# Kernel tuning notes

Measured on AMD Instinct MI355X. Metric: run time of the kernel, lower is better.

## Reference

```python
import jax, jax.numpy as jnp
import numpy as np

D_MODEL = 1024
NUM_HEADS = 16
D_HEAD = D_MODEL // NUM_HEADS
NEG_BIG = 10000000000.0  # matches the torch module's -1e10 mask constant


def setup_inputs() -> dict:
    key = jax.random.key(0)
    ks = jax.random.split(key, 9)
    d = D_MODEL
    scale = 1.0 / np.sqrt(d)
    inp = {
        "x": jax.random.normal(ks[0], (2, 2048, d), dtype=jnp.float32),
        "W_q": jax.random.normal(ks[1], (d, d), dtype=jnp.float32) * scale,
        "b_q": jnp.zeros((d,), dtype=jnp.float32),
        "W_k": jax.random.normal(ks[2], (d, d), dtype=jnp.float32) * scale,
        "b_k": jnp.zeros((d,), dtype=jnp.float32),
        "W_v": jax.random.normal(ks[3], (d, d), dtype=jnp.float32) * scale,
        "b_v": jnp.zeros((d,), dtype=jnp.float32),
        "W_o": jax.random.normal(ks[4], (d, d), dtype=jnp.float32) * scale,
        "b_o": jnp.zeros((d,), dtype=jnp.float32),
    }
    return inp


def reference(x, W_q, b_q, W_k, b_k, W_v, b_v, W_o, b_o):
    B, S, d = x.shape
    H, Dh = NUM_HEADS, D_HEAD

    Q = x @ W_q + b_q  # [B,S,d]
    K = x @ W_k + b_k
    V = x @ W_v + b_v

    # split heads: [B,S,d] -> [B,H,S,Dh]
    Qh = Q.reshape(B, S, H, Dh).transpose(0, 2, 1, 3)
    Kh = K.reshape(B, S, H, Dh).transpose(0, 2, 1, 3)
    Vh = V.reshape(B, S, H, Dh).transpose(0, 2, 1, 3)

    scores = jnp.einsum("bhid,bhjd->bhij", Qh, Kh) / jnp.sqrt(
        jnp.asarray(Dh, dtype=x.dtype)
    )

    # causal mask: tril(scores) - 1e10 * (1 - tril_mask)
    causal = jnp.tril(jnp.ones((S, S), dtype=x.dtype))
    scores = scores * causal - NEG_BIG * (1.0 - causal)

    attn = jax.nn.softmax(scores, axis=-1)  # dropout p=0.0 -> identity

    vals = jnp.einsum("bhij,bhjd->bhid", attn, Vh)  # [B,H,S,Dh]
    vals = vals.transpose(0, 2, 1, 3).reshape(B, S, d)

    return vals @ W_o + b_o
```

## Files before the change

### kernel.cpp

```cpp
#include <hip/hip_runtime.h>

typedef unsigned short u16;
typedef __attribute__((ext_vector_type(8))) short short8;
typedef __attribute__((ext_vector_type(4))) short shortx4;
typedef __attribute__((ext_vector_type(4))) float floatx4;

#define S_ 2048
#define D_ 1024
#define DQKV_ 3072
#define H_ 16
#define DH_ 64

#define EXP2F(x) __builtin_amdgcn_exp2f(x)

__device__ __forceinline__ float bf2f(u16 x) {
    union { unsigned int u; float f; } v; v.u = ((unsigned int)x) << 16; return v.f;
}
__device__ __forceinline__ u16 f2bf(float f) {
    unsigned int u = __float_as_uint(f);
    return (u16)((u + 0x7fffu + ((u >> 16) & 1u)) >> 16);
}
__device__ __forceinline__ u16 f2bf_fast(float f) {
    return (u16)((__float_as_uint(f) + 0x8000u) >> 16);
}

__device__ __forceinline__ void async16(const void* g, void* l) {
    __builtin_amdgcn_global_load_lds(
        (const __attribute__((address_space(1))) unsigned int*)g,
        (__attribute__((address_space(3))) unsigned int*)l, 16, 0, 0);
}

__global__ __launch_bounds__(256) void convert_x(const float* __restrict__ x, u16* __restrict__ xb) {
    const size_t i = ((size_t)blockIdx.x * 256 + threadIdx.x) * 4;
    float4 v = *(const float4*)&x[i];
    shortx4 h;
    h[0] = (short)f2bf(v.x); h[1] = (short)f2bf(v.y);
    h[2] = (short)f2bf(v.z); h[3] = (short)f2bf(v.w);
    *(shortx4*)&xb[i] = h;
}

__global__ __launch_bounds__(256) void transpose_w4(const float* __restrict__ Wq, const float* __restrict__ Wk,
                                                    const float* __restrict__ Wv, const float* __restrict__ Wo,
                                                    u16* __restrict__ Wqkvt, u16* __restrict__ Wot) {
    __shared__ u16 tile[32][33];
    const int z = blockIdx.z;
    const float* W = (z == 0) ? Wq : (z == 1) ? Wk : (z == 2) ? Wv : Wo;
    u16* dst = (z == 3) ? Wot : (Wqkvt + (size_t)z * D_ * D_);
    const int tx = threadIdx.x, ty = threadIdx.y;
    const int n0 = blockIdx.x * 32, k0 = blockIdx.y * 32;
#pragma unroll
    for (int r = 0; r < 4; ++r) {
        int k = ty + r * 8;
        tile[k][tx] = f2bf(W[(size_t)(k0 + k) * D_ + n0 + tx]);
    }
    __syncthreads();
#pragma unroll
    for (int r = 0; r < 4; ++r) {
        int n = ty + r * 8;
        dst[(size_t)(n0 + n) * D_ + k0 + tx] = tile[tx][n];
    }
}

__global__ __launch_bounds__(256) void transpose_headV(const u16* __restrict__ QKV, u16* __restrict__ Vt) {
    __shared__ u16 tile[64 * 65];
    const int t = threadIdx.x;
    const int bh = blockIdx.y, b = bh >> 4, h = bh & 15;
    const int s0 = blockIdx.x << 6;
#pragma unroll
    for (int i = 0; i < 16; ++i) {
        int idx = t + (i << 8);
        int s = idx >> 6, d = idx & 63;
        tile[s * 65 + d] = QKV[(size_t)(b * S_ + s0 + s) * DQKV_ + 2048 + h * DH_ + d];
    }
    __syncthreads();
#pragma unroll
    for (int i = 0; i < 16; ++i) {
        int idx = t + (i << 8);
        int d = idx >> 6, s = idx & 63;
        Vt[((size_t)bh * DH_ + d) * S_ + s0 + s] = tile[s * 65 + d];
    }
}

template <int BM, int BN, bool OUTF32>
__global__ __launch_bounds__(256) void gemm_bt(const u16* __restrict__ A, const u16* __restrict__ Bt,
                                               const float* __restrict__ b0, const float* __restrict__ b1,
                                               const float* __restrict__ b2, void* __restrict__ Cp,
                                               int M, int N, int Kd) {
    constexpr int FI = BM / 32, FJ = BN / 32;
    __shared__ __align__(16) u16 As[2][BM * 32];
    __shared__ __align__(16) u16 Bs[2][BN * 32];
    const int t = threadIdx.x;
    const int m0 = blockIdx.y * BM, n0 = blockIdx.x * BN;
    const int w = t >> 6, lane = t & 63;
    const int lr = lane & 15, lg = lane >> 4;
    const int wm = (w >> 1) * (BM / 2), wn = (w & 1) * (BN / 2);
    const int srow = lane >> 2, scol = (lane & 3) << 3;
    floatx4 acc[FI][FJ] = {};

    auto stage = [&](int buf, int k0) {
#pragma unroll
        for (int c = 0; c < BM / 64; ++c) {
            int rbase = (w * (BM / 64) + c) * 16;
            async16(&A[(size_t)(m0 + rbase + srow) * Kd + k0 + scol], &As[buf][rbase * 32]);
        }
#pragma unroll
        for (int c = 0; c < BN / 64; ++c) {
            int rbase = (w * (BN / 64) + c) * 16;
            async16(&Bt[(size_t)(n0 + rbase + srow) * Kd + k0 + scol], &Bs[buf][rbase * 32]);
        }
    };

    stage(0, 0);
    const int nk = Kd / 32;
    for (int kk = 0; kk < nk; ++kk) {
        const int cur = kk & 1;
        __syncthreads();
        if (kk + 1 < nk) stage(cur ^ 1, (kk + 1) * 32);

        short8 af[FI], bfr[FJ];
#pragma unroll
        for (int i = 0; i < FI; ++i) af[i]  = *(const short8*)&As[cur][(wm + i * 16 + lr) * 32 + lg * 8];
#pragma unroll
        for (int j = 0; j < FJ; ++j) bfr[j] = *(const short8*)&Bs[cur][(wn + j * 16 + lr) * 32 + lg * 8];
#pragma unroll
        for (int i = 0; i < FI; ++i)
#pragma unroll
            for (int j = 0; j < FJ; ++j)
                acc[i][j] = __builtin_amdgcn_mfma_f32_16x16x32_bf16(af[i], bfr[j], acc[i][j], 0, 0, 0);
    }

#pragma unroll
    for (int j = 0; j < FJ; ++j) {
        int col = n0 + wn + j * 16 + lr;
        const float* bp = (col < 1024) ? b0 : (col < 2048) ? b1 : b2;
        float bv = bp[col & 1023];
#pragma unroll
        for (int i = 0; i < FI; ++i) {
            int rb = m0 + wm + i * 16 + lg * 4;
#pragma unroll
            for (int ii = 0; ii < 4; ++ii) {
                float val = acc[i][j][ii] + bv;
                if (OUTF32) ((float*)Cp)[(size_t)(rb + ii) * N + col] = val;
                else        ((u16*)Cp)[(size_t)(rb + ii) * N + col] = f2bf(val);
            }
        }
    }
}

__global__ __launch_bounds__(256) void attn_mfma(const u16* __restrict__ QKV, const u16* __restrict__ Vt,
                                                 u16* __restrict__ O) {
    __shared__ __align__(16) u16 KsA[2][64 * 64];
    __shared__ __align__(16) u16 VsA[2][64 * 64];
    __shared__ __align__(16) u16 Ps[4 * 16 * 64];
    const int t = threadIdx.x, w = t >> 6, lane = t & 63;
    const int lr = lane & 15, lg = lane >> 4;
    const int bh = blockIdx.x, b = bh >> 4, h = bh & 15;
    const int qt = 31 - blockIdx.y;
    const int q0 = qt << 6;
    const float cs = 0.18033688f;

    const u16* Kb  = QKV + (size_t)b * S_ * DQKV_ + 1024 + h * DH_;
    const u16* Vtb = Vt + (size_t)bh * DH_ * S_;
    u16* Pw = Ps + w * (16 * 64);

    const int rb = lane >> 3;
    const int cc = ((lane & 7) ^ rb) << 3;
    const int swz = lr & 7;

    short8 qf[2];
#pragma unroll
    for (int ks = 0; ks < 2; ++ks)
        qf[ks] = *(const short8*)&QKV[(size_t)(b * S_ + q0 + w * 16 + lr) * DQKV_ + h * DH_ + ks * 32 + lg * 8];

    floatx4 of[4] = {};
    float lsum[4] = {0.f, 0.f, 0.f, 0.f};

    {
        u16* Kd = &KsA[0][w * 512];
        u16* Vd = &VsA[0][w * 512];
        async16(&Kb[(size_t)(w * 8 + rb) * DQKV_ + cc], Kd);
        async16(&Kb[(size_t)(32 + w * 8 + rb) * DQKV_ + cc], Kd + 2048);
        async16(&Vtb[(size_t)(w * 8 + rb) * S_ + cc], Vd);
        async16(&Vtb[(size_t)(32 + w * 8 + rb) * S_ + cc], Vd + 2048);
    }

    for (int kb = 0; kb <= qt; ++kb) {
        const int cur = kb & 1;
        __syncthreads();
        if (kb < qt) {
            const int K1 = (kb + 1) << 6;
            u16* Kd = &KsA[cur ^ 1][w * 512];
            u16* Vd = &VsA[cur ^ 1][w * 512];
            async16(&Kb[(size_t)(K1 + w * 8 + rb) * DQKV_ + cc], Kd);
            async16(&Kb[(size_t)(K1 + 32 + w * 8 + rb) * DQKV_ + cc], Kd + 2048);
            async16(&Vtb[(size_t)(w * 8 + rb) * S_ + K1 + cc], Vd);
            async16(&Vtb[(size_t)(32 + w * 8 + rb) * S_ + K1 + cc], Vd + 2048);
        }
        const u16* Kc = KsA[cur];
        const u16* Vc = VsA[cur];

        floatx4 sf[4] = {};
#pragma unroll
        for (int ks = 0; ks < 2; ++ks)
#pragma unroll
            for (int j = 0; j < 4; ++j) {
                short8 kf = *(const short8*)&Kc[(j * 16 + lr) * 64 + ((((ks << 2) + lg) ^ swz) << 3)];
                sf[j] = __builtin_amdgcn_mfma_f32_16x16x32_bf16(qf[ks], kf, sf[j], 0, 0, 0);
            }

        const bool diag = (kb == qt);
#pragma unroll
        for (int j = 0; j < 4; ++j)
#pragma unroll
            for (int ii = 0; ii < 4; ++ii) {
                float ev = EXP2F(sf[j][ii] * cs);
                if (diag && (j * 16 + lr > w * 16 + lg * 4 + ii)) ev = 0.f;
                lsum[ii] += ev;
                int r = lg * 4 + ii;
                int chunk = ((j * 2 + (lr >> 3)) ^ (r & 7));
                Pw[r * 64 + (chunk << 3) + (lr & 7)] = f2bf_fast(ev);
            }

#pragma unroll
        for (int ks = 0; ks < 2; ++ks) {
            short8 pa = *(const short8*)&Pw[lr * 64 + ((((ks << 2) + lg) ^ swz) << 3)];
#pragma unroll
            for (int j = 0; j < 4; ++j) {
                short8 vf = *(const short8*)&Vc[(j * 16 + lr) * 64 + ((((ks << 2) + lg) ^ swz) << 3)];
                of[j] = __builtin_amdgcn_mfma_f32_16x16x32_bf16(pa, vf, of[j], 0, 0, 0);
            }
        }
    }

    float rinv[4];
#pragma unroll
    for (int ii = 0; ii < 4; ++ii) {
        float s = lsum[ii];
#pragma unroll
        for (int off = 1; off < 16; off <<= 1) s += __shfl_xor(s, off);
        rinv[ii] = 1.f / s;
    }
#pragma unroll
    for (int j = 0; j < 4; ++j)
#pragma unroll
        for (int ii = 0; ii < 4; ++ii)
            O[(size_t)(b * S_ + q0 + w * 16 + lg * 4 + ii) * D_ + h * DH_ + j * 16 + lr] =
                f2bf(of[j][ii] * rinv[ii]);
}

extern "C" void kernel_launch(void* const* d_in, const int* in_sizes, int n_in,
                              void* d_out, int out_size, void* d_ws, size_t ws_size,
                              hipStream_t stream) {
    (void)in_sizes; (void)n_in; (void)out_size; (void)ws_size;
    const float* x  = (const float*)d_in[0];
    const float* Wq = (const float*)d_in[1];
    const float* bq = (const float*)d_in[2];
    const float* Wk = (const float*)d_in[3];
    const float* bk = (const float*)d_in[4];
    const float* Wv = (const float*)d_in[5];
    const float* bv = (const float*)d_in[6];
    const float* Wo = (const float*)d_in[7];
    const float* bo = (const float*)d_in[8];

    u16* ws    = (u16*)d_ws;
    u16* WqkvT = ws;
    u16* WoT   = ws + (size_t)3 * (1 << 20);
    u16* QKV   = ws + (size_t)4 * (1 << 20);
    u16* Vtm   = ws + (size_t)16 * (1 << 20);
    u16* xbf   = ws + (size_t)20 * (1 << 20);
    u16* Am    = ws + (size_t)20 * (1 << 20);

    convert_x<<<4096, 256, 0, stream>>>(x, xbf);
    transpose_w4<<<dim3(32, 32, 4), dim3(32, 8), 0, stream>>>(Wq, Wk, Wv, Wo, WqkvT, WoT);

    gemm_bt<128, 128, false><<<dim3(DQKV_ / 128, 4096 / 128), 256, 0, stream>>>(
        xbf, WqkvT, bq, bk, bv, QKV, 4096, DQKV_, 1024);

    transpose_headV<<<dim3(32, 32), 256, 0, stream>>>(QKV, Vtm);

    attn_mfma<<<dim3(32, 32), 256, 0, stream>>>(QKV, Vtm, Am);

    gemm_bt<64, 128, true><<<dim3(1024 / 128, 4096 / 64), 256, 0, stream>>>(
        Am, WoT, bo, bo, bo, d_out, 4096, 1024, 1024);
}
```

Measured before the change: 191.0 us.

## Double attention query tile to 128 rows and fuse x conversion into weight prep

```diff
diff --git a/kernel.cpp b/kernel.cpp
--- a/kernel.cpp
+++ b/kernel.cpp
@@ -30,20 +30,27 @@
         (__attribute__((address_space(3))) unsigned int*)l, 16, 0, 0);
 }
 
-__global__ __launch_bounds__(256) void convert_x(const float* __restrict__ x, u16* __restrict__ xb) {
-    const size_t i = ((size_t)blockIdx.x * 256 + threadIdx.x) * 4;
-    float4 v = *(const float4*)&x[i];
-    shortx4 h;
-    h[0] = (short)f2bf(v.x); h[1] = (short)f2bf(v.y);
-    h[2] = (short)f2bf(v.z); h[3] = (short)f2bf(v.w);
-    *(shortx4*)&xb[i] = h;
-}
-
-__global__ __launch_bounds__(256) void transpose_w4(const float* __restrict__ Wq, const float* __restrict__ Wk,
-                                                    const float* __restrict__ Wv, const float* __restrict__ Wo,
-                                                    u16* __restrict__ Wqkvt, u16* __restrict__ Wot) {
+__global__ __launch_bounds__(256) void prep_w(const float* __restrict__ Wq, const float* __restrict__ Wk,
+                                              const float* __restrict__ Wv, const float* __restrict__ Wo,
+                                              const float* __restrict__ x,
+                                              u16* __restrict__ Wqkvt, u16* __restrict__ Wot,
+                                              u16* __restrict__ xb) {
+    const int z = blockIdx.z;
+    const int t = threadIdx.y * 32 + threadIdx.x;
+    if (z == 4) {
+        const size_t base = (size_t)(blockIdx.y * 32 + blockIdx.x) * 4096;
+#pragma unroll
+        for (int r = 0; r < 4; ++r) {
+            size_t i = base + ((size_t)(r * 256 + t)) * 4;
+            float4 v = *(const float4*)&x[i];
+            shortx4 hh;
+            hh[0] = (short)f2bf(v.x); hh[1] = (short)f2bf(v.y);
+            hh[2] = (short)f2bf(v.z); hh[3] = (short)f2bf(v.w);
+            *(shortx4*)&xb[i] = hh;
+        }
+        return;
+    }
     __shared__ u16 tile[32][33];
-    const int z = blockIdx.z;
     const float* W = (z == 0) ? Wq : (z == 1) ? Wk : (z == 2) ? Wv : Wo;
     u16* dst = (z == 3) ? Wot : (Wqkvt + (size_t)z * D_ * D_);
     const int tx = threadIdx.x, ty = threadIdx.y;
@@ -151,29 +158,32 @@
                                                  u16* __restrict__ O) {
     __shared__ __align__(16) u16 KsA[2][64 * 64];
     __shared__ __align__(16) u16 VsA[2][64 * 64];
-    __shared__ __align__(16) u16 Ps[4 * 16 * 64];
+    __shared__ __align__(16) u16 Ps[4][2][16 * 32];
     const int t = threadIdx.x, w = t >> 6, lane = t & 63;
     const int lr = lane & 15, lg = lane >> 4;
     const int bh = blockIdx.x, b = bh >> 4, h = bh & 15;
-    const int qt = 31 - blockIdx.y;
-    const int q0 = qt << 6;
+    const int qt = 15 - blockIdx.y;
+    const int q0 = qt << 7;
     const float cs = 0.18033688f;
 
     const u16* Kb  = QKV + (size_t)b * S_ * DQKV_ + 1024 + h * DH_;
     const u16* Vtb = Vt + (size_t)bh * DH_ * S_;
-    u16* Pw = Ps + w * (16 * 64);
 
     const int rb = lane >> 3;
     const int cc = ((lane & 7) ^ rb) << 3;
     const int swz = lr & 7;
-
-    short8 qf[2];
-#pragma unroll
-    for (int ks = 0; ks < 2; ++ks)
-        qf[ks] = *(const short8*)&QKV[(size_t)(b * S_ + q0 + w * 16 + lr) * DQKV_ + h * DH_ + ks * 32 + lg * 8];
-
-    floatx4 of[4] = {};
-    float lsum[4] = {0.f, 0.f, 0.f, 0.f};
+    const int pswz = (lr >> 2) & 3;
+
+    short8 qf[2][2];
+#pragma unroll
+    for (int mi = 0; mi < 2; ++mi)
+#pragma unroll
+        for (int ks = 0; ks < 2; ++ks)
+            qf[mi][ks] = *(const short8*)&QKV[(size_t)(b * S_ + q0 + mi * 64 + w * 16 + lr) * DQKV_ +
+                                              h * DH_ + ks * 32 + lg * 8];
+
+    floatx4 of0[4] = {}, of1[4] = {};
+    float ls0[4] = {0.f, 0.f, 0.f, 0.f}, ls1[4] = {0.f, 0.f, 0.f, 0.f};
 
     {
         u16* Kd = &KsA[0][w * 512];
@@ -184,10 +194,11 @@
         async16(&Vtb[(size_t)(32 + w * 8 + rb) * S_ + cc], Vd + 2048);
     }
 
-    for (int kb = 0; kb <= qt; ++kb) {
+    const int nkb = 2 * qt + 2;
+    for (int kb = 0; kb < nkb; ++kb) {
         const int cur = kb & 1;
         __syncthreads();
-        if (kb < qt) {
+        if (kb + 1 < nkb) {
             const int K1 = (kb + 1) << 6;
             u16* Kd = &KsA[cur ^ 1][w * 512];
             u16* Vd = &VsA[cur ^ 1][w * 512];
@@ -198,54 +209,81 @@
         }
         const u16* Kc = KsA[cur];
         const u16* Vc = VsA[cur];
-
-        floatx4 sf[4] = {};
-#pragma unroll
-        for (int ks = 0; ks < 2; ++ks)
-#pragma unroll
-            for (int j = 0; j < 4; ++j) {
-                short8 kf = *(const short8*)&Kc[(j * 16 + lr) * 64 + ((((ks << 2) + lg) ^ swz) << 3)];
-                sf[j] = __builtin_amdgcn_mfma_f32_16x16x32_bf16(qf[ks], kf, sf[j], 0, 0, 0);
+        u16* P0 = &Ps[w][0][0];
+        u16* P1 = &Ps[w][1][0];
+
+        const bool act0  = (kb + 1 < nkb);
+        const bool mask0 = (kb == nkb - 2);
+        const bool mask1 = (kb == nkb - 1);
+
+#pragma unroll
+        for (int jp = 0; jp < 2; ++jp) {
+            floatx4 s00 = {}, s01 = {}, s10 = {}, s11 = {};
+#pragma unroll
+            for (int ks = 0; ks < 2; ++ks) {
+                const int co = (((ks << 2) + lg) ^ swz) << 3;
+                short8 kfa = *(const short8*)&Kc[(jp * 32 + lr) * 64 + co];
+                short8 kfb = *(const short8*)&Kc[(jp * 32 + 16 + lr) * 64 + co];
+                if (act0) {
+                    s00 = __builtin_amdgcn_mfma_f32_16x16x32_bf16(qf[0][ks], kfa, s00, 0, 0, 0);
+                    s01 = __builtin_amdgcn_mfma_f32_16x16x32_bf16(qf[0][ks], kfb, s01, 0, 0, 0);
+                }
+                s10 = __builtin_amdgcn_mfma_f32_16x16x32_bf16(qf[1][ks], kfa, s10, 0, 0, 0);
+                s11 = __builtin_amdgcn_mfma_f32_16x16x32_bf16(qf[1][ks], kfb, s11, 0, 0, 0);
             }
-
-        const bool diag = (kb == qt);
-#pragma unroll
-        for (int j = 0; j < 4; ++j)
-#pragma unroll
-            for (int ii = 0; ii < 4; ++ii) {
-                float ev = EXP2F(sf[j][ii] * cs);
-                if (diag && (j * 16 + lr > w * 16 + lg * 4 + ii)) ev = 0.f;
-                lsum[ii] += ev;
-                int r = lg * 4 + ii;
-                int chunk = ((j * 2 + (lr >> 3)) ^ (r & 7));
-                Pw[r * 64 + (chunk << 3) + (lr & 7)] = f2bf_fast(ev);
+            const int colbase = kb * 64 + jp * 32;
+#pragma unroll
+            for (int jl = 0; jl < 2; ++jl) {
+                const int keyloc = jl * 16 + lr;
+                const int colg = colbase + keyloc;
+                const floatx4 sa0 = jl ? s01 : s00;
+                const floatx4 sa1 = jl ? s11 : s10;
+#pragma unroll
+                for (int ii = 0; ii < 4; ++ii) {
+                    const int r = lg * 4 + ii;
+                    const int addr = r * 32 + ((((keyloc >> 3) ^ ((r >> 2) & 3)) << 3) | (keyloc & 7));
+                    if (act0) {
+                        float e0 = EXP2F(sa0[ii] * cs);
+                        if (mask0 && colg > q0 + w * 16 + r) e0 = 0.f;
+                        ls0[ii] += e0;
+                        P0[addr] = f2bf_fast(e0);
+                    }
+                    float e1 = EXP2F(sa1[ii] * cs);
+                    if (mask1 && colg > q0 + 64 + w * 16 + r) e1 = 0.f;
+                    ls1[ii] += e1;
+                    P1[addr] = f2bf_fast(e1);
+                }
             }
-
-#pragma unroll
-        for (int ks = 0; ks < 2; ++ks) {
-            short8 pa = *(const short8*)&Pw[lr * 64 + ((((ks << 2) + lg) ^ swz) << 3)];
-#pragma unroll
-            for (int j = 0; j < 4; ++j) {
-                short8 vf = *(const short8*)&Vc[(j * 16 + lr) * 64 + ((((ks << 2) + lg) ^ swz) << 3)];
-                of[j] = __builtin_amdgcn_mfma_f32_16x16x32_bf16(pa, vf, of[j], 0, 0, 0);
+            const int paddr = lr * 32 + ((lg ^ pswz) << 3);
+            short8 pa0 = *(const short8*)&P0[paddr];
+            short8 pa1 = *(const short8*)&P1[paddr];
+            const int co2 = (((jp << 2) + lg) ^ swz) << 3;
+#pragma unroll
+            for (int j2 = 0; j2 < 4; ++j2) {
+                short8 vf = *(const short8*)&Vc[(j2 * 16 + lr) * 64 + co2];
+                if (act0) of0[j2] = __builtin_amdgcn_mfma_f32_16x16x32_bf16(pa0, vf, of0[j2], 0, 0, 0);
+                of1[j2] = __builtin_amdgcn_mfma_f32_16x16x32_bf16(pa1, vf, of1[j2], 0, 0, 0);
             }
         }
     }
 
-    float rinv[4];
+    float r0[4], r1[4];
 #pragma unroll
     for (int ii = 0; ii < 4; ++ii) {
-        float s = lsum[ii];
-#pragma unroll
-        for (int off = 1; off < 16; off <<= 1) s += __shfl_xor(s, off);
-        rinv[ii] = 1.f / s;
+        float s0 = ls0[ii], s1 = ls1[ii];
+#pragma unroll
+        for (int off = 1; off < 16; off <<= 1) { s0 += __shfl_xor(s0, off); s1 += __shfl_xor(s1, off); }
+        r0[ii] = 1.f / s0; r1[ii] = 1.f / s1;
     }
 #pragma unroll
     for (int j = 0; j < 4; ++j)
 #pragma unroll
-        for (int ii = 0; ii < 4; ++ii)
+        for (int ii = 0; ii < 4; ++ii) {
             O[(size_t)(b * S_ + q0 + w * 16 + lg * 4 + ii) * D_ + h * DH_ + j * 16 + lr] =
-                f2bf(of[j][ii] * rinv[ii]);
+                f2bf(of0[j][ii] * r0[ii]);
+            O[(size_t)(b * S_ + q0 + 64 + w * 16 + lg * 4 + ii) * D_ + h * DH_ + j * 16 + lr] =
+                f2bf(of1[j][ii] * r1[ii]);
+        }
 }
 
 extern "C" void kernel_launch(void* const* d_in, const int* in_sizes, int n_in,
@@ -270,15 +308,14 @@
     u16* xbf   = ws + (size_t)20 * (1 << 20);
     u16* Am    = ws + (size_t)20 * (1 << 20);
 
-    convert_x<<<4096, 256, 0, stream>>>(x, xbf);
-    transpose_w4<<<dim3(32, 32, 4), dim3(32, 8), 0, stream>>>(Wq, Wk, Wv, Wo, WqkvT, WoT);
+    prep_w<<<dim3(32, 32, 5), dim3(32, 8), 0, stream>>>(Wq, Wk, Wv, Wo, x, WqkvT, WoT, xbf);
 
     gemm_bt<128, 128, false><<<dim3(DQKV_ / 128, 4096 / 128), 256, 0, stream>>>(
         xbf, WqkvT, bq, bk, bv, QKV, 4096, DQKV_, 1024);
 
     transpose_headV<<<dim3(32, 32), 256, 0, stream>>>(QKV, Vtm);
 
-    attn_mfma<<<dim3(32, 32), 256, 0, stream>>>(QKV, Vtm, Am);
+    attn_mfma<<<dim3(32, 16), 256, 0, stream>>>(QKV, Vtm, Am);
 
     gemm_bt<64, 128, true><<<dim3(1024 / 128, 4096 / 64), 256, 0, stream>>>(
         Am, WoT, bo, bo, bo, d_out, 4096, 1024, 1024);
```

After: 229.2 us. 20.0% more time.
